# Kernel optimization log

Hardware: AMD Instinct MI355X
Metric: run time of the kernel (lower is better)

The kernel has to match this reference:

```python
import jax, jax.numpy as jnp
import numpy as np

ENC_D, PRED_D, JOINT_D, VOCAB = 256, 256, 512, 1024

def setup_inputs() -> dict:
    key = jax.random.key(0)
    ks = jax.random.split(key, 8)
    B, T, U = 4, 256, 64
    s = lambda d: 1.0 / np.sqrt(d)
    return {
        "encoder_outputs": jax.random.normal(ks[0], (B, T, ENC_D), jnp.float32),
        "predictor_outputs": jax.random.normal(ks[1], (B, U, PRED_D), jnp.float32),
        "W_enc": jax.random.uniform(ks[2], (ENC_D, JOINT_D), jnp.float32, -s(ENC_D), s(ENC_D)),
        "b_enc": jax.random.uniform(ks[3], (JOINT_D,), jnp.float32, -s(ENC_D), s(ENC_D)),
        "W_dec": jax.random.uniform(ks[4], (PRED_D, JOINT_D), jnp.float32, -s(PRED_D), s(PRED_D)),
        "b_dec": jax.random.uniform(ks[5], (JOINT_D,), jnp.float32, -s(PRED_D), s(PRED_D)),
        "W_out": jax.random.uniform(ks[6], (JOINT_D, VOCAB), jnp.float32, -s(JOINT_D), s(JOINT_D)),
        "b_out": jax.random.uniform(ks[7], (VOCAB,), jnp.float32, -s(JOINT_D), s(JOINT_D)),
    }

def reference(encoder_outputs, predictor_outputs, W_enc, b_enc, W_dec, b_dec, W_out, b_out):
    # [B,T,J] and [B,U,J] projections
    enc = jnp.einsum('bte,ej->btj', encoder_outputs, W_enc) + b_enc
    pred = jnp.einsum('bup,pj->buj', predictor_outputs, W_dec) + b_dec
    # broadcast add -> [B,T,U,J], tanh, then output projection -> [B,T,U,V]
    joint = jnp.tanh(enc[:, :, None, :] + pred[:, None, :, :])
    logits = jnp.einsum('btuj,jv->btuv', joint, W_out) + b_out
    return logits
```

## Files before the change

### kernel.cpp

```cpp
#include <hip/hip_runtime.h>
#include <hip/hip_bf16.h>

typedef __attribute__((ext_vector_type(8))) short bf16x8;
typedef __attribute__((ext_vector_type(4))) float f32x4;
typedef __attribute__((ext_vector_type(4))) float fvec4;
typedef __attribute__((ext_vector_type(8))) unsigned short u16x8;


__device__ __forceinline__ unsigned short f2bf(float f) {
  unsigned int u = __builtin_bit_cast(unsigned int, f);
  u += 0x7FFFu + ((u >> 16) & 1u);
  return (unsigned short)(u >> 16);
}

__device__ __forceinline__ float fast_tanh(float x) {
  float cx = fminf(fmaxf(x, -9.0f), 9.0f);
  float e2 = __expf(cx + cx);
  return (e2 - 1.0f) * __builtin_amdgcn_rcpf(e2 + 1.0f);
}


__device__ __forceinline__ void proj_body(
    const float* __restrict__ x, const float* __restrict__ W,
    const float* __restrict__ bias, float* __restrict__ out,
    int blk, uint8_t* sh) {
  float (*xt)[9] = (float (*)[9])sh;
  const int tid = threadIdx.x;
  const int row0 = blk << 3;
  #pragma unroll
  for (int i = 0; i < 8; ++i)
    xt[tid][i] = x[(size_t)(row0 + i) * 256 + tid];
  __syncthreads();
  float acc0[8] = {0.f,0.f,0.f,0.f,0.f,0.f,0.f,0.f};
  float acc1[8] = {0.f,0.f,0.f,0.f,0.f,0.f,0.f,0.f};
  #pragma unroll 4
  for (int k = 0; k < 256; ++k) {
    float w0 = W[(size_t)k * 512 + tid];
    float w1 = W[(size_t)k * 512 + tid + 256];
    #pragma unroll
    for (int r = 0; r < 8; ++r) {
      float xv = xt[k][r];
      acc0[r] = fmaf(xv, w0, acc0[r]);
      acc1[r] = fmaf(xv, w1, acc1[r]);
    }
  }
  float b0 = bias[tid], b1 = bias[tid + 256];
  #pragma unroll
  for (int r = 0; r < 8; ++r) {
    out[(size_t)(row0 + r) * 512 + tid]       = acc0[r] + b0;
    out[(size_t)(row0 + r) * 512 + tid + 256] = acc1[r] + b1;
  }
}

__device__ __forceinline__ void transpose_body(
    const float* __restrict__ W, unsigned short* __restrict__ Bt2,
    int blk, uint8_t* sh) {
  unsigned short (*tile)[65] = (unsigned short (*)[65])sh;
  const int k0 = (blk & 7) << 6;
  const int n0 = (blk >> 3) << 6;
  const int tid = threadIdx.x;
  #pragma unroll
  for (int i = 0; i < 16; ++i) {
    int idx = tid + (i << 8);
    int r = idx >> 6, c = idx & 63;
    tile[r][c] = f2bf(W[(size_t)(k0 + r) * 1024 + n0 + c]);
  }
  __syncthreads();
  #pragma unroll
  for (int i = 0; i < 16; ++i) {
    int idx = tid + (i << 8);
    int r = idx >> 6, c = idx & 63;
    int ng = n0 + r, kg = k0 + c;
    size_t dst = ((size_t)(ng >> 9) << 18) + ((size_t)(kg >> 5) << 14)
               + ((ng & 511) << 5) + (kg & 31);
    Bt2[dst] = tile[c][r];
  }
}

__global__ __launch_bounds__(256) void prep_kernel(
    const float* __restrict__ enc, const float* __restrict__ We,
    const float* __restrict__ be, float* __restrict__ encp,
    const float* __restrict__ pred, const float* __restrict__ Wd,
    const float* __restrict__ bd, float* __restrict__ predp,
    const float* __restrict__ Wo, unsigned short* __restrict__ Bt2) {
  __shared__ uint8_t sh[9216];
  const int b = blockIdx.x;
  if (b < 128)       proj_body(enc, We, be, encp, b, sh);
  else if (b < 160)  proj_body(pred, Wd, bd, predp, b - 128, sh);
  else               transpose_body(Wo, Bt2, b - 160, sh);
}

__global__ __launch_bounds__(512, 4) void fused_gemm(
    const float* __restrict__ encp, const float* __restrict__ predp,
    const unsigned short* __restrict__ Bt2, const float* __restrict__ bout,
    float* __restrict__ out) {
  __shared__ uint8_t lds[66560];
  const int tid = threadIdx.x;
  const int lane = tid & 63, wid = tid >> 6;
  const int fr = lane & 15, fg = lane >> 4;
  const int b = blockIdx.x;
  const int wg = ((b & 7) << 8) + (b >> 3);
  const int mt = wg >> 1, half = wg & 1;
  const int m0 = mt << 6;
  const int cb0 = half << 9;

  const unsigned short* Bgl =
      Bt2 + ((size_t)half << 18) + (((wid << 6) + fr) << 5) + (fg << 3);

  bf16x8 bA[4], bB[4];
  #pragma unroll
  for (int nf = 0; nf < 4; ++nf)
    bA[nf] = *(const bf16x8*)(Bgl + (nf << 9));

  {
    const int r = tid >> 3, cb = tid & 7;
    const float* erow = encp + ((size_t)mt << 9);
    const float* prow = predp + ((size_t)(((mt >> 8) << 6) + r) << 9);
    uint8_t* rowbase = lds + (r << 10);
    #pragma unroll
    for (int c8 = 0; c8 < 8; ++c8) {
      int chunk = cb + (c8 << 3);
      int k8 = chunk << 3;
      fvec4 e0 = *(const fvec4*)(erow + k8);
      fvec4 e1 = *(const fvec4*)(erow + k8 + 4);
      fvec4 p0 = *(const fvec4*)(prow + k8);
      fvec4 p1 = *(const fvec4*)(prow + k8 + 4);
      u16x8 o;
      #pragma unroll
      for (int i = 0; i < 4; ++i) o[i]     = f2bf(fast_tanh(e0[i] + p0[i]));
      #pragma unroll
      for (int i = 0; i < 4; ++i) o[i + 4] = f2bf(fast_tanh(e1[i] + p1[i]));
      *(u16x8*)(rowbase + ((chunk ^ (r & 7)) << 4)) = o;
    }
  }
  asm volatile("s_waitcnt lgkmcnt(0)" ::: "memory");
  __builtin_amdgcn_s_barrier();

  f32x4 acc[4][4];
  f32x4 zero4 = {0.f, 0.f, 0.f, 0.f};
  #pragma unroll
  for (int i = 0; i < 4; ++i)
    #pragma unroll
    for (int j = 0; j < 4; ++j) acc[i][j] = zero4;

  const int qh = (fr >> 2) & 1;
  int arow[4];
  #pragma unroll
  for (int mf = 0; mf < 4; ++mf)
    arow[mf] = ((((mf << 4) + fr)) << 10) + ((fg ^ (fr & 3)) << 4);

  auto step = [&](int kt, bf16x8 (&cur)[4], bf16x8 (&nxt)[4]) {
    const int ktn = kt < 15 ? kt + 1 : 15;
    #pragma unroll
    for (int nf = 0; nf < 4; ++nf)
      nxt[nf] = *(const bf16x8*)(Bgl + (ktn << 14) + (nf << 9));
    const int ko = (kt ^ qh) << 6;
    bf16x8 af[4];
    #pragma unroll
    for (int mf = 0; mf < 4; ++mf)
      af[mf] = *(const bf16x8*)(lds + arow[mf] + ko);
    #pragma unroll
    for (int mf = 0; mf < 4; ++mf)
      #pragma unroll
      for (int nf = 0; nf < 4; ++nf)
        acc[mf][nf] = __builtin_amdgcn_mfma_f32_16x16x32_bf16(cur[nf], af[mf],
                                                              acc[mf][nf], 0, 0, 0);
  };

  #pragma unroll
  for (int kt = 0; kt < 16; kt += 2) {
    step(kt,     bA, bB);
    step(kt + 1, bB, bA);
  }

  const int colw = (wid << 6) + (fg << 2);
  fvec4 bvv[4];
  #pragma unroll
  for (int nf = 0; nf < 4; ++nf)
    bvv[nf] = *(const fvec4*)&bout[cb0 + colw + (nf << 4)];

  #pragma unroll
  for (int mf = 0; mf < 4; ++mf) {
    float* ep = (float*)(lds + (mf & 1) * 33024);
    asm volatile("s_waitcnt lgkmcnt(0)" ::: "memory");
    __builtin_amdgcn_s_barrier();
    #pragma unroll
    for (int nf = 0; nf < 4; ++nf) {
      fvec4 o = acc[mf][nf] + bvv[nf];
      *(fvec4*)&ep[fr * 516 + colw + (nf << 4)] = o;
    }
    asm volatile("s_waitcnt lgkmcnt(0)" ::: "memory");
    __builtin_amdgcn_s_barrier();
    #pragma unroll
    for (int j = 0; j < 4; ++j) {
      const int idx = (wid << 2) + j;
      const int row = idx >> 1, seg = idx & 1;
      fvec4 v = *(const fvec4*)&ep[row * 516 + (seg << 8) + (lane << 2)];
      __builtin_nontemporal_store(
          v, (fvec4*)&out[(size_t)(m0 + (mf << 4) + row) * 1024 + cb0 +
                          (seg << 8) + (lane << 2)]);
    }
  }
}

extern "C" void kernel_launch(void* const* d_in, const int* in_sizes, int n_in,
                              void* d_out, int out_size, void* d_ws, size_t ws_size,
                              hipStream_t stream) {
  const float* enc   = (const float*)d_in[0];
  const float* pred  = (const float*)d_in[1];
  const float* W_enc = (const float*)d_in[2];
  const float* b_enc = (const float*)d_in[3];
  const float* W_dec = (const float*)d_in[4];
  const float* b_dec = (const float*)d_in[5];
  const float* W_out = (const float*)d_in[6];
  const float* b_out = (const float*)d_in[7];
  float* out = (float*)d_out;

  uint8_t* ws = (uint8_t*)d_ws;
  float* encp  = (float*)ws;
  float* predp = (float*)(ws + 2097152);
  unsigned short* bt2 = (unsigned short*)(ws + 2621440);

  prep_kernel<<<288, 256, 0, stream>>>(enc, W_enc, b_enc, encp,
                                       pred, W_dec, b_dec, predp,
                                       W_out, bt2);
  fused_gemm<<<2048, 512, 0, stream>>>(encp, predp, bt2, b_out, out);
}
```

Measured before the change: 125.2 us.

## Switch fused GEMM from 16x16x32 to 32x32x16 bf16 MFMA tiles

Replaces the 16x16x32 MFMA tiling with 32x32x16 instructions, using 2x2 accumulator fragments of 16 floats per wave. The packed W_out layout changes to 16-wide k-groups, and the LDS swizzle of the tanh activations widens to 16 chunks to match. The epilogue is rewritten to stage 32-row blocks through LDS before the nontemporal stores. The aim is fewer MFMA issues and fewer operand loads per FLOP. In exchange it doubles the number of k-steps and changes the LDS access patterns.

```diff
diff --git a/kernel.cpp b/kernel.cpp
--- a/kernel.cpp
+++ b/kernel.cpp
@@ -2,8 +2,8 @@
 #include <hip/hip_bf16.h>
 
 typedef __attribute__((ext_vector_type(8))) short bf16x8;
-typedef __attribute__((ext_vector_type(4))) float f32x4;
 typedef __attribute__((ext_vector_type(4))) float fvec4;
+typedef __attribute__((ext_vector_type(16))) float f32x16;
 typedef __attribute__((ext_vector_type(8))) unsigned short u16x8;
 
 
@@ -53,7 +53,7 @@
 }
 
 __device__ __forceinline__ void transpose_body(
-    const float* __restrict__ W, unsigned short* __restrict__ Bt2,
+    const float* __restrict__ W, unsigned short* __restrict__ Bt3,
     int blk, uint8_t* sh) {
   unsigned short (*tile)[65] = (unsigned short (*)[65])sh;
   const int k0 = (blk & 7) << 6;
@@ -71,9 +71,9 @@
     int idx = tid + (i << 8);
     int r = idx >> 6, c = idx & 63;
     int ng = n0 + r, kg = k0 + c;
-    size_t dst = ((size_t)(ng >> 9) << 18) + ((size_t)(kg >> 5) << 14)
-               + ((ng & 511) << 5) + (kg & 31);
-    Bt2[dst] = tile[c][r];
+    size_t dst = ((size_t)(ng >> 9) << 18) + ((size_t)(kg >> 4) << 13)
+               + ((ng & 511) << 4) + (kg & 15);
+    Bt3[dst] = tile[c][r];
   }
 }
 
@@ -82,22 +82,22 @@
     const float* __restrict__ be, float* __restrict__ encp,
     const float* __restrict__ pred, const float* __restrict__ Wd,
     const float* __restrict__ bd, float* __restrict__ predp,
-    const float* __restrict__ Wo, unsigned short* __restrict__ Bt2) {
+    const float* __restrict__ Wo, unsigned short* __restrict__ Bt3) {
   __shared__ uint8_t sh[9216];
   const int b = blockIdx.x;
   if (b < 128)       proj_body(enc, We, be, encp, b, sh);
   else if (b < 160)  proj_body(pred, Wd, bd, predp, b - 128, sh);
-  else               transpose_body(Wo, Bt2, b - 160, sh);
+  else               transpose_body(Wo, Bt3, b - 160, sh);
 }
 
 __global__ __launch_bounds__(512, 4) void fused_gemm(
     const float* __restrict__ encp, const float* __restrict__ predp,
-    const unsigned short* __restrict__ Bt2, const float* __restrict__ bout,
+    const unsigned short* __restrict__ Bt3, const float* __restrict__ bout,
     float* __restrict__ out) {
   __shared__ uint8_t lds[66560];
   const int tid = threadIdx.x;
   const int lane = tid & 63, wid = tid >> 6;
-  const int fr = lane & 15, fg = lane >> 4;
+  const int l31 = lane & 31, hi = lane >> 5;
   const int b = blockIdx.x;
   const int wg = ((b & 7) << 8) + (b >> 3);
   const int mt = wg >> 1, half = wg & 1;
@@ -105,12 +105,12 @@
   const int cb0 = half << 9;
 
   const unsigned short* Bgl =
-      Bt2 + ((size_t)half << 18) + (((wid << 6) + fr) << 5) + (fg << 3);
-
-  bf16x8 bA[4], bB[4];
-  #pragma unroll
-  for (int nf = 0; nf < 4; ++nf)
-    bA[nf] = *(const bf16x8*)(Bgl + (nf << 9));
+      Bt3 + ((size_t)half << 18) + (((wid << 6) + l31) << 4) + (hi << 3);
+
+  bf16x8 bA[2], bB[2];
+  #pragma unroll
+  for (int na = 0; na < 2; ++na)
+    bA[na] = *(const bf16x8*)(Bgl + (na << 9));
 
   {
     const int r = tid >> 3, cb = tid & 7;
@@ -130,75 +130,82 @@
       for (int i = 0; i < 4; ++i) o[i]     = f2bf(fast_tanh(e0[i] + p0[i]));
       #pragma unroll
       for (int i = 0; i < 4; ++i) o[i + 4] = f2bf(fast_tanh(e1[i] + p1[i]));
-      *(u16x8*)(rowbase + ((chunk ^ (r & 7)) << 4)) = o;
+      *(u16x8*)(rowbase + ((chunk ^ (r & 15)) << 4)) = o;
     }
   }
   asm volatile("s_waitcnt lgkmcnt(0)" ::: "memory");
   __builtin_amdgcn_s_barrier();
 
-  f32x4 acc[4][4];
-  f32x4 zero4 = {0.f, 0.f, 0.f, 0.f};
-  #pragma unroll
-  for (int i = 0; i < 4; ++i)
-    #pragma unroll
-    for (int j = 0; j < 4; ++j) acc[i][j] = zero4;
-
-  const int qh = (fr >> 2) & 1;
-  int arow[4];
-  #pragma unroll
-  for (int mf = 0; mf < 4; ++mf)
-    arow[mf] = ((((mf << 4) + fr)) << 10) + ((fg ^ (fr & 3)) << 4);
-
-  auto step = [&](int kt, bf16x8 (&cur)[4], bf16x8 (&nxt)[4]) {
-    const int ktn = kt < 15 ? kt + 1 : 15;
-    #pragma unroll
-    for (int nf = 0; nf < 4; ++nf)
-      nxt[nf] = *(const bf16x8*)(Bgl + (ktn << 14) + (nf << 9));
-    const int ko = (kt ^ qh) << 6;
-    bf16x8 af[4];
-    #pragma unroll
-    for (int mf = 0; mf < 4; ++mf)
-      af[mf] = *(const bf16x8*)(lds + arow[mf] + ko);
-    #pragma unroll
-    for (int mf = 0; mf < 4; ++mf)
-      #pragma unroll
-      for (int nf = 0; nf < 4; ++nf)
-        acc[mf][nf] = __builtin_amdgcn_mfma_f32_16x16x32_bf16(cur[nf], af[mf],
-                                                              acc[mf][nf], 0, 0, 0);
+  f32x16 acc[2][2];
+  #pragma unroll
+  for (int i = 0; i < 2; ++i)
+    #pragma unroll
+    for (int j = 0; j < 2; ++j)
+      #pragma unroll
+      for (int e = 0; e < 16; ++e) acc[i][j][e] = 0.f;
+
+  const int hx = hi ^ (lane & 15);
+  int arowb[2];
+  #pragma unroll
+  for (int ma = 0; ma < 2; ++ma)
+    arowb[ma] = ((ma << 5) + l31) << 10;
+
+  auto step = [&](int kt, bf16x8 (&cur)[2], bf16x8 (&nxt)[2]) {
+    const int ktn = kt < 31 ? kt + 1 : 31;
+    #pragma unroll
+    for (int na = 0; na < 2; ++na)
+      nxt[na] = *(const bf16x8*)(Bgl + (ktn << 13) + (na << 9));
+    const int ao = (((kt << 1) ^ hx) << 4);
+    bf16x8 af[2];
+    #pragma unroll
+    for (int ma = 0; ma < 2; ++ma)
+      af[ma] = *(const bf16x8*)(lds + arowb[ma] + ao);
+    #pragma unroll
+    for (int ma = 0; ma < 2; ++ma)
+      #pragma unroll
+      for (int na = 0; na < 2; ++na)
+        acc[ma][na] = __builtin_amdgcn_mfma_f32_32x32x16_bf16(
+            cur[na], af[ma], acc[ma][na], 0, 0, 0);
   };
 
   #pragma unroll
-  for (int kt = 0; kt < 16; kt += 2) {
+  for (int kt = 0; kt < 32; kt += 2) {
     step(kt,     bA, bB);
     step(kt + 1, bB, bA);
   }
 
-  const int colw = (wid << 6) + (fg << 2);
-  fvec4 bvv[4];
-  #pragma unroll
-  for (int nf = 0; nf < 4; ++nf)
-    bvv[nf] = *(const fvec4*)&bout[cb0 + colw + (nf << 4)];
-
-  #pragma unroll
-  for (int mf = 0; mf < 4; ++mf) {
-    float* ep = (float*)(lds + (mf & 1) * 33024);
+  float (*epi)[516] = (float (*)[516])lds;
+  fvec4 bvv[2][4];
+  #pragma unroll
+  for (int na = 0; na < 2; ++na)
+    #pragma unroll
+    for (int q = 0; q < 4; ++q)
+      bvv[na][q] = *(const fvec4*)&bout[cb0 + (wid << 6) + (na << 5) +
+                                       (q << 3) + (hi << 2)];
+
+  #pragma unroll
+  for (int ma = 0; ma < 2; ++ma) {
     asm volatile("s_waitcnt lgkmcnt(0)" ::: "memory");
     __builtin_amdgcn_s_barrier();
     #pragma unroll
-    for (int nf = 0; nf < 4; ++nf) {
-      fvec4 o = acc[mf][nf] + bvv[nf];
-      *(fvec4*)&ep[fr * 516 + colw + (nf << 4)] = o;
-    }
+    for (int na = 0; na < 2; ++na)
+      #pragma unroll
+      for (int q = 0; q < 4; ++q) {
+        fvec4 o;
+        #pragma unroll
+        for (int j = 0; j < 4; ++j) o[j] = acc[ma][na][(q << 2) + j] + bvv[na][q][j];
+        *(fvec4*)&epi[l31][(wid << 6) + (na << 5) + (q << 3) + (hi << 2)] = o;
+      }
     asm volatile("s_waitcnt lgkmcnt(0)" ::: "memory");
     __builtin_amdgcn_s_barrier();
     #pragma unroll
-    for (int j = 0; j < 4; ++j) {
-      const int idx = (wid << 2) + j;
+    for (int j = 0; j < 8; ++j) {
+      const int idx = (wid << 3) + j;
       const int row = idx >> 1, seg = idx & 1;
-      fvec4 v = *(const fvec4*)&ep[row * 516 + (seg << 8) + (lane << 2)];
+      fvec4 v = *(const fvec4*)&epi[row][(seg << 8) + (lane << 2)];
+      const int gm = m0 + (ma << 5) + row;
       __builtin_nontemporal_store(
-          v, (fvec4*)&out[(size_t)(m0 + (mf << 4) + row) * 1024 + cb0 +
-                          (seg << 8) + (lane << 2)]);
+          v, (fvec4*)&out[(size_t)gm * 1024 + cb0 + (seg << 8) + (lane << 2)]);
     }
   }
 }
@@ -219,10 +226,10 @@
   uint8_t* ws = (uint8_t*)d_ws;
   float* encp  = (float*)ws;
   float* predp = (float*)(ws + 2097152);
-  unsigned short* bt2 = (unsigned short*)(ws + 2621440);
+  unsigned short* bt3 = (unsigned short*)(ws + 2621440);
 
   prep_kernel<<<288, 256, 0, stream>>>(enc, W_enc, b_enc, encp,
                                        pred, W_dec, b_dec, predp,
-                                       W_out, bt2);
-  fused_gemm<<<2048, 512, 0, stream>>>(encp, predp, bt2, b_out, out);
-}
+                                       W_out, bt3);
+  fused_gemm<<<2048, 512, 0, stream>>>(encp, predp, bt3, b_out, out);
+}
```

New measurement: 126.3 us. About the same (+0.9%).
